# Optimization experiments

Hardware: AMD Instinct MI355X
Metric: run time of the kernel (lower is better)

The kernel has to match this reference:

```python
import jax, jax.numpy as jnp
import numpy as np

NUM_USERS = 100000
NUM_ITEMS = 50000
N = NUM_USERS + NUM_ITEMS
EMB = 64
NNZ = 4000000
B = 4096
GAMMA = 1.0
REG_LAMBDA = 1e-4
T_END = 1.0  # Euler step size: t = [0, 1]
EPS = 1e-12


def setup_inputs() -> dict:
    key = jax.random.key(0)
    ks = jax.random.split(key, 8)
    user = jax.random.randint(ks[0], (B,), 0, NUM_USERS)
    positive = jax.random.randint(ks[1], (B,), 0, NUM_ITEMS)
    negative = jax.random.randint(ks[2], (B,), 0, NUM_ITEMS)
    adj_rows = jax.random.randint(ks[3], (NNZ,), 0, N)
    adj_cols = jax.random.randint(ks[4], (NNZ,), 0, N)
    # normalized-adjacency-like small positive values
    adj_vals = jax.random.uniform(ks[5], (NNZ,), jnp.float32) * 1e-3
    user_emb = jax.random.normal(ks[6], (NUM_USERS, EMB), jnp.float32) * 0.1
    item_emb = jax.random.normal(ks[7], (NUM_ITEMS, EMB), jnp.float32) * 0.1
    return {
        "user": user, "positive": positive, "negative": negative,
        "adj_rows": adj_rows, "adj_cols": adj_cols, "adj_vals": adj_vals,
        "user_emb": user_emb, "item_emb": item_emb,
    }


def _normalize(x):
    return x * jax.lax.rsqrt(jnp.sum(x * x, axis=-1, keepdims=True) + EPS)


def _uniform_loss(x):
    # log mean_{i<j} exp(-2 * ||xn_i - xn_j||^2), xn = L2-normalized
    xn = _normalize(x)
    sq = jnp.maximum(2.0 - 2.0 * (xn @ xn.T), 0.0)  # [B, B] pairwise squared dist
    mask = jnp.triu(jnp.ones((x.shape[0], x.shape[0]), bool), k=1)
    vals = jnp.where(mask, jnp.exp(-2.0 * sq), 0.0)
    n_pairs = x.shape[0] * (x.shape[0] - 1) / 2.0
    return jnp.log(jnp.sum(vals) / n_pairs)


def reference(user, positive, negative, adj_rows, adj_cols, adj_vals, user_emb, item_emb):
    # ego embeddings: concat user/item tables -> [N, EMB]
    x = jnp.concatenate([user_emb, item_emb], axis=0)
    # sparse spmm: ax = A @ x (COO gather + segment reduce)
    ax = jax.ops.segment_sum(adj_vals[:, None] * x[adj_cols], adj_rows, num_segments=N)
    # ODEFunc f(t, x) = A@x + e with e = x0; one Euler step z1 = x0 + t*(A@x0 + x0)
    z = x + T_END * (ax + x)
    u_all, i_all = z[:NUM_USERS], z[NUM_USERS:]
    u = u_all[user]          # [B, EMB]
    i = i_all[positive]      # [B, EMB]
    # alignment loss on normalized embeddings
    un, inn = _normalize(u), _normalize(i)
    align = jnp.mean(jnp.sum((un - inn) ** 2, axis=-1))
    # uniformity loss
    uniform = GAMMA * (_uniform_loss(u) + _uniform_loss(i)) / 2.0
    # L2 reg on ego (pre-propagation) embeddings
    ego_u = user_emb[user]
    ego_i = item_emb[positive]
    reg = REG_LAMBDA * 0.5 * (jnp.sum(ego_u ** 2) + jnp.sum(ego_i ** 2)) / B
    return jnp.stack([align, uniform, reg])
```

## Files before the change

### kernel.cpp

```cpp
#include <hip/hip_runtime.h>
#include <math.h>

#define NUSERS 100000
#define NITEMS 50000
#define NN (NUSERS + NITEMS)
#define EMB 64
#define NNZ_ 4000000
#define BB 4096
#define NSLOT (2 * BB)
#define CAP 128
#define FSTR 32
#define BMW 4688
#define EPSN 1e-12f
#define NT128 32


typedef __attribute__((ext_vector_type(8))) short short8v;
typedef __attribute__((ext_vector_type(16))) float f32x16;

__device__ inline float wave_reduce_sum(float v) {
  #pragma unroll
  for (int off = 32; off >= 1; off >>= 1) v += __shfl_xor(v, off, 64);
  return v;
}

__device__ inline unsigned short f2bf(float f) {
  unsigned u = __float_as_uint(f);
  unsigned r = u + 0x7fffu + ((u >> 16) & 1u);
  return (unsigned short)(r >> 16);
}

__global__ __launch_bounds__(256) void lg_init(int* map, int* fillp, unsigned* bitmap) {
  int t = blockIdx.x * blockDim.x + threadIdx.x;
  if (t < NN) map[t] = -1;
  if (t < NSLOT * FSTR) fillp[t] = 0;
  if (t < BMW) bitmap[t] = 0u;
}

__global__ __launch_bounds__(256) void lg_mark(const int* __restrict__ user,
                                               const int* __restrict__ positive,
                                               int* __restrict__ map,
                                               unsigned* __restrict__ bitmap) {
  int t = blockIdx.x * blockDim.x + threadIdx.x;
  if (t >= 2 * BB) return;
  int row = (t < BB) ? user[t] : (NUSERS + positive[t - BB]);
  atomicCAS(&map[row], -1, t);
  atomicOr(&bitmap[row >> 5], 1u << (row & 31));
}

__device__ inline void lg_bin_one(int r, int c, float v, const unsigned* bm,
                                  const int* map, int* fillp, uint2* bins) {
  if ((bm[r >> 5] >> (r & 31)) & 1u) {
    int s = map[r];
    int pos = atomicAdd(&fillp[s * FSTR], 1);
    if (pos < CAP) {
      uint2 e; e.x = (unsigned)c; e.y = __float_as_uint(v);
      bins[(size_t)s * CAP + pos] = e;
    }
  }
}

__global__ __launch_bounds__(256) void lg_scan_bin(const int4* __restrict__ rows4,
                                                   const int4* __restrict__ cols4,
                                                   const float4* __restrict__ vals4,
                                                   const unsigned* __restrict__ bitmap,
                                                   const int* __restrict__ map,
                                                   int* __restrict__ fillp,
                                                   uint2* __restrict__ bins) {
  __shared__ unsigned bm[BMW];
  for (int i = threadIdx.x; i < BMW; i += 256) bm[i] = bitmap[i];
  __syncthreads();
  const int ngroups = NNZ_ / 4;
  for (int g = blockIdx.x * 256 + threadIdx.x; g < ngroups; g += gridDim.x * 256) {
    int4 r = rows4[g];
    int4 c = cols4[g];
    float4 v = vals4[g];
    lg_bin_one(r.x, c.x, v.x, bm, map, fillp, bins);
    lg_bin_one(r.y, c.y, v.y, bm, map, fillp, bins);
    lg_bin_one(r.z, c.z, v.z, bm, map, fillp, bins);
    lg_bin_one(r.w, c.w, v.w, bm, map, fillp, bins);
  }
}

__global__ __launch_bounds__(256) void lg_accum(const int* __restrict__ fillp,
                                                const uint2* __restrict__ bins,
                                                const float* __restrict__ uemb,
                                                const float* __restrict__ iemb,
                                                float* __restrict__ acc) {
  int w = (blockIdx.x * blockDim.x + threadIdx.x) >> 6;
  int lane = threadIdx.x & 63;
  if (w >= NSLOT) return;
  int n = min(fillp[w * FSTR], CAP);
  const uint2* bs = bins + (size_t)w * CAP;
  float a = 0.0f;
  int k = 0;
  for (; k + 4 <= n; k += 4) {
    uint2 e0 = bs[k];
    uint2 e1 = bs[k + 1];
    uint2 e2 = bs[k + 2];
    uint2 e3 = bs[k + 3];
    int c0 = (int)e0.x; float v0 = __uint_as_float(e0.y);
    int c1 = (int)e1.x; float v1 = __uint_as_float(e1.y);
    int c2 = (int)e2.x; float v2 = __uint_as_float(e2.y);
    int c3 = (int)e3.x; float v3 = __uint_as_float(e3.y);
    const float* x0 = (c0 < NUSERS) ? uemb + (size_t)c0 * EMB : iemb + (size_t)(c0 - NUSERS) * EMB;
    const float* x1 = (c1 < NUSERS) ? uemb + (size_t)c1 * EMB : iemb + (size_t)(c1 - NUSERS) * EMB;
    const float* x2 = (c2 < NUSERS) ? uemb + (size_t)c2 * EMB : iemb + (size_t)(c2 - NUSERS) * EMB;
    const float* x3 = (c3 < NUSERS) ? uemb + (size_t)c3 * EMB : iemb + (size_t)(c3 - NUSERS) * EMB;
    float f0 = x0[lane], f1 = x1[lane], f2 = x2[lane], f3 = x3[lane];
    a = fmaf(v0, f0, a);
    a = fmaf(v1, f1, a);
    a = fmaf(v2, f2, a);
    a = fmaf(v3, f3, a);
  }
  for (; k < n; ++k) {
    uint2 e0 = bs[k];
    int c0 = (int)e0.x; float v0 = __uint_as_float(e0.y);
    const float* x0 = (c0 < NUSERS) ? uemb + (size_t)c0 * EMB : iemb + (size_t)(c0 - NUSERS) * EMB;
    a = fmaf(v0, x0[lane], a);
  }
  acc[(size_t)w * EMB + lane] = a;
}

__global__ __launch_bounds__(256) void lg_prep(const int* __restrict__ user,
                                               const int* __restrict__ positive,
                                               const float* __restrict__ uemb,
                                               const float* __restrict__ iemb,
                                               const int* __restrict__ map,
                                               const float* __restrict__ acc,
                                               unsigned short* __restrict__ zub,
                                               unsigned short* __restrict__ zib,
                                               float* __restrict__ part_align,
                                               float* __restrict__ part_reg) {
  int w = (blockIdx.x * blockDim.x + threadIdx.x) >> 6;
  int lane = threadIdx.x & 63;
  if (w >= BB) return;
  int ru = user[w];
  int pi = positive[w];
  float eu = uemb[(size_t)ru * EMB + lane];
  float ei = iemb[(size_t)pi * EMB + lane];
  int su = map[ru];
  int si = map[NUSERS + pi];
  float zul = 2.0f * eu + acc[(size_t)su * EMB + lane];
  float zil = 2.0f * ei + acc[(size_t)si * EMB + lane];
  float nu = wave_reduce_sum(zul * zul);
  float ni = wave_reduce_sum(zil * zil);
  float un = zul * rsqrtf(nu + EPSN);
  float inn = zil * rsqrtf(ni + EPSN);
  zub[(size_t)w * EMB + lane] = f2bf(un);
  zib[(size_t)w * EMB + lane] = f2bf(inn);
  float d = un - inn;
  float align_b = wave_reduce_sum(d * d);
  float reg_b = wave_reduce_sum(eu * eu + ei * ei);
  if (lane == 0) {
    part_align[w] = align_b;
    part_reg[w] = reg_b;
  }
}

__global__ __launch_bounds__(256) void lg_gram_mfma(const unsigned short* __restrict__ zub,
                                                    const unsigned short* __restrict__ zib,
                                                    float* __restrict__ gpart) {
  int jb = blockIdx.x, ib = blockIdx.y, m = blockIdx.z;
  int bid = (m << 10) + (ib << 5) + jb;
  if (jb < ib) {
    if (threadIdx.x == 0) gpart[bid] = 0.0f;
    return;
  }
  const unsigned short* z = (m == 0) ? zub : zib;
  __shared__ float wsum[4];
  int t = threadIdx.x;
  int l = t & 63, w = t >> 6;
  int wr = w >> 1, wc = w & 1;
  int lr = l & 31;
  int koff = (l >> 5) * 8;
  const short8v* pa0 = (const short8v*)(z + (size_t)(ib * 128 + wr * 64 + lr) * EMB + koff);
  const short8v* pa1 = (const short8v*)(z + (size_t)(ib * 128 + wr * 64 + 32 + lr) * EMB + koff);
  const short8v* pb0 = (const short8v*)(z + (size_t)(jb * 128 + wc * 64 + lr) * EMB + koff);
  const short8v* pb1 = (const short8v*)(z + (size_t)(jb * 128 + wc * 64 + 32 + lr) * EMB + koff);
  f32x16 a00 = {}, a01 = {}, a10 = {}, a11 = {};
  #pragma unroll
  for (int ks = 0; ks < 4; ++ks) {
    short8v a0 = pa0[ks * 2];
    short8v a1 = pa1[ks * 2];
    short8v b0 = pb0[ks * 2];
    short8v b1 = pb1[ks * 2];
    a00 = __builtin_amdgcn_mfma_f32_32x32x16_bf16(a0, b0, a00, 0, 0, 0);
    a01 = __builtin_amdgcn_mfma_f32_32x32x16_bf16(a0, b1, a01, 0, 0, 0);
    a10 = __builtin_amdgcn_mfma_f32_32x32x16_bf16(a1, b0, a10, 0, 0, 0);
    a11 = __builtin_amdgcn_mfma_f32_32x32x16_bf16(a1, b1, a11, 0, 0, 0);
  }
  float s = 0.0f;
  #pragma unroll
  for (int e = 0; e < 16; ++e) {
    float v0 = a00[e], v1 = a01[e], v2 = a10[e], v3 = a11[e];
    s += __expf(-2.0f * fmaxf(fmaf(-2.0f, v0, 2.0f), 0.0f));
    s += __expf(-2.0f * fmaxf(fmaf(-2.0f, v1, 2.0f), 0.0f));
    s += __expf(-2.0f * fmaxf(fmaf(-2.0f, v2, 2.0f), 0.0f));
    s += __expf(-2.0f * fmaxf(fmaf(-2.0f, v3, 2.0f), 0.0f));
  }
  s = wave_reduce_sum(s);
  if (l == 0) wsum[w] = s;
  __syncthreads();
  if (t == 0) {
    float tot = wsum[0] + wsum[1] + wsum[2] + wsum[3];
    float wgt = (ib == jb) ? 1.0f : 2.0f;
    gpart[bid] = wgt * tot;
  }
}

__global__ __launch_bounds__(256) void lg_final(const float* __restrict__ part_align,
                                                const float* __restrict__ part_reg,
                                                const float* __restrict__ gpart,
                                                float* __restrict__ out) {
  __shared__ float red[4][4];
  int t = threadIdx.x;
  float sa = 0.0f, sr = 0.0f, su = 0.0f, si = 0.0f;
  for (int k = t; k < 4096; k += 256) {
    sa += part_align[k];
    sr += part_reg[k];
  }
  for (int k = t; k < 1024; k += 256) {
    su += gpart[k];
    si += gpart[1024 + k];
  }
  sa = wave_reduce_sum(sa);
  sr = wave_reduce_sum(sr);
  su = wave_reduce_sum(su);
  si = wave_reduce_sum(si);
  if ((t & 63) == 0) {
    int wid = t >> 6;
    red[wid][0] = sa; red[wid][1] = sr; red[wid][2] = su; red[wid][3] = si;
  }
  __syncthreads();
  if (t == 0) {
    float a = 0, r = 0, Su = 0, Si = 0;
    #pragma unroll
    for (int wv = 0; wv < 4; ++wv) {
      a += red[wv][0]; r += red[wv][1]; Su += red[wv][2]; Si += red[wv][3];
    }
    float align = a / (float)BB;
    float reg = 1e-4f * 0.5f * r / (float)BB;
    float npairs = (float)BB * (float)(BB - 1) * 0.5f;
    float tri_u = (Su - (float)BB) * 0.5f;
    float tri_i = (Si - (float)BB) * 0.5f;
    float Lu = logf(tri_u / npairs);
    float Li = logf(tri_i / npairs);
    out[0] = align;
    out[1] = 0.5f * (Lu + Li);
    out[2] = reg;
  }
}

extern "C" void kernel_launch(void* const* d_in, const int* in_sizes, int n_in,
                              void* d_out, int out_size, void* d_ws, size_t ws_size,
                              hipStream_t stream) {
  const int* user = (const int*)d_in[0];
  const int* positive = (const int*)d_in[1];
  const int* adj_rows = (const int*)d_in[3];
  const int* adj_cols = (const int*)d_in[4];
  const float* adj_vals = (const float*)d_in[5];
  const float* uemb = (const float*)d_in[6];
  const float* iemb = (const float*)d_in[7];

  char* ws = (char*)d_ws;
  int* map = (int*)(ws);
  int* fillp = (int*)(ws + (1u << 20));
  uint2* bins = (uint2*)(ws + (2u << 20));
  float* acc = (float*)(ws + (10u << 20));
  unsigned short* zub = (unsigned short*)(ws + (12u << 20));
  unsigned short* zib = (unsigned short*)(ws + (12u << 20) + (512u << 10));
  float* part_align = (float*)(ws + (13u << 20));
  float* part_reg = (float*)(ws + (13u << 20) + (16u << 10));
  float* gpart = (float*)(ws + (13u << 20) + (32u << 10));
  unsigned* bitmap = (unsigned*)(ws + (13u << 20) + (64u << 10));
  float* out = (float*)d_out;

  lg_init<<<dim3(1024), dim3(256), 0, stream>>>(map, fillp, bitmap);
  lg_mark<<<dim3(32), dim3(256), 0, stream>>>(user, positive, map, bitmap);
  lg_scan_bin<<<dim3(2048), dim3(256), 0, stream>>>(
      (const int4*)adj_rows, (const int4*)adj_cols, (const float4*)adj_vals,
      bitmap, map, fillp, bins);
  lg_accum<<<dim3(NSLOT / 4), dim3(256), 0, stream>>>(fillp, bins, uemb, iemb, acc);
  lg_prep<<<dim3(1024), dim3(256), 0, stream>>>(user, positive, uemb, iemb, map,
                                                acc, zub, zib, part_align, part_reg);
  lg_gram_mfma<<<dim3(NT128, NT128, 2), dim3(256), 0, stream>>>(zub, zib, gpart);
  lg_final<<<dim3(1), dim3(256), 0, stream>>>(part_align, part_reg, gpart, out);
}
```

Measured before the change: 71.79 us.

## Scan only row indices when binning; gather cols/vals later; enlarge Gram tiles

The binning scan now streams only adj_rows and stores the edge index for each matching entry. The later accumulate kernel gathers the column and value for those few edges, which removes two full 16MB streams from the scan. The Gram kernel moves to 256x256 upper-triangle tiles with 512 threads, indexed over 136 triangle blocks so no blocks launch only to exit. The cost is an extra dependent indirect load per edge in the accumulate step and fewer, larger Gram blocks.

```diff
diff --git a/kernel.cpp b/kernel.cpp
--- a/kernel.cpp
+++ b/kernel.cpp
@@ -12,7 +12,9 @@
 #define FSTR 32
 #define BMW 4688
 #define EPSN 1e-12f
-#define NT128 32
+#define BT 256
+#define NTB 16
+#define NTRI 136
 
 
 typedef __attribute__((ext_vector_type(8))) short short8v;
@@ -48,42 +50,38 @@
   atomicOr(&bitmap[row >> 5], 1u << (row & 31));
 }
 
-__device__ inline void lg_bin_one(int r, int c, float v, const unsigned* bm,
-                                  const int* map, int* fillp, uint2* bins) {
+__device__ inline void lg_bin_one(int r, int k, const unsigned* bm,
+                                  const int* map, int* fillp, unsigned* binsk) {
   if ((bm[r >> 5] >> (r & 31)) & 1u) {
     int s = map[r];
     int pos = atomicAdd(&fillp[s * FSTR], 1);
-    if (pos < CAP) {
-      uint2 e; e.x = (unsigned)c; e.y = __float_as_uint(v);
-      bins[(size_t)s * CAP + pos] = e;
-    }
+    if (pos < CAP) binsk[(size_t)s * CAP + pos] = (unsigned)k;
   }
 }
 
 __global__ __launch_bounds__(256) void lg_scan_bin(const int4* __restrict__ rows4,
-                                                   const int4* __restrict__ cols4,
-                                                   const float4* __restrict__ vals4,
                                                    const unsigned* __restrict__ bitmap,
                                                    const int* __restrict__ map,
                                                    int* __restrict__ fillp,
-                                                   uint2* __restrict__ bins) {
+                                                   unsigned* __restrict__ binsk) {
   __shared__ unsigned bm[BMW];
   for (int i = threadIdx.x; i < BMW; i += 256) bm[i] = bitmap[i];
   __syncthreads();
   const int ngroups = NNZ_ / 4;
   for (int g = blockIdx.x * 256 + threadIdx.x; g < ngroups; g += gridDim.x * 256) {
     int4 r = rows4[g];
-    int4 c = cols4[g];
-    float4 v = vals4[g];
-    lg_bin_one(r.x, c.x, v.x, bm, map, fillp, bins);
-    lg_bin_one(r.y, c.y, v.y, bm, map, fillp, bins);
-    lg_bin_one(r.z, c.z, v.z, bm, map, fillp, bins);
-    lg_bin_one(r.w, c.w, v.w, bm, map, fillp, bins);
+    int kb = g * 4;
+    lg_bin_one(r.x, kb + 0, bm, map, fillp, binsk);
+    lg_bin_one(r.y, kb + 1, bm, map, fillp, binsk);
+    lg_bin_one(r.z, kb + 2, bm, map, fillp, binsk);
+    lg_bin_one(r.w, kb + 3, bm, map, fillp, binsk);
   }
 }
 
 __global__ __launch_bounds__(256) void lg_accum(const int* __restrict__ fillp,
-                                                const uint2* __restrict__ bins,
+                                                const unsigned* __restrict__ binsk,
+                                                const int* __restrict__ cols,
+                                                const float* __restrict__ vals,
                                                 const float* __restrict__ uemb,
                                                 const float* __restrict__ iemb,
                                                 float* __restrict__ acc) {
@@ -91,18 +89,15 @@
   int lane = threadIdx.x & 63;
   if (w >= NSLOT) return;
   int n = min(fillp[w * FSTR], CAP);
-  const uint2* bs = bins + (size_t)w * CAP;
+  const unsigned* bs = binsk + (size_t)w * CAP;
   float a = 0.0f;
   int k = 0;
   for (; k + 4 <= n; k += 4) {
-    uint2 e0 = bs[k];
-    uint2 e1 = bs[k + 1];
-    uint2 e2 = bs[k + 2];
-    uint2 e3 = bs[k + 3];
-    int c0 = (int)e0.x; float v0 = __uint_as_float(e0.y);
-    int c1 = (int)e1.x; float v1 = __uint_as_float(e1.y);
-    int c2 = (int)e2.x; float v2 = __uint_as_float(e2.y);
-    int c3 = (int)e3.x; float v3 = __uint_as_float(e3.y);
+    unsigned k0 = bs[k], k1 = bs[k + 1], k2 = bs[k + 2], k3 = bs[k + 3];
+    int c0 = cols[k0]; float v0 = vals[k0];
+    int c1 = cols[k1]; float v1 = vals[k1];
+    int c2 = cols[k2]; float v2 = vals[k2];
+    int c3 = cols[k3]; float v3 = vals[k3];
     const float* x0 = (c0 < NUSERS) ? uemb + (size_t)c0 * EMB : iemb + (size_t)(c0 - NUSERS) * EMB;
     const float* x1 = (c1 < NUSERS) ? uemb + (size_t)c1 * EMB : iemb + (size_t)(c1 - NUSERS) * EMB;
     const float* x2 = (c2 < NUSERS) ? uemb + (size_t)c2 * EMB : iemb + (size_t)(c2 - NUSERS) * EMB;
@@ -114,8 +109,8 @@
     a = fmaf(v3, f3, a);
   }
   for (; k < n; ++k) {
-    uint2 e0 = bs[k];
-    int c0 = (int)e0.x; float v0 = __uint_as_float(e0.y);
+    unsigned k0 = bs[k];
+    int c0 = cols[k0]; float v0 = vals[k0];
     const float* x0 = (c0 < NUSERS) ? uemb + (size_t)c0 * EMB : iemb + (size_t)(c0 - NUSERS) * EMB;
     a = fmaf(v0, x0[lane], a);
   }
@@ -158,54 +153,68 @@
   }
 }
 
-__global__ __launch_bounds__(256) void lg_gram_mfma(const unsigned short* __restrict__ zub,
+__global__ __launch_bounds__(512) void lg_gram_mfma(const unsigned short* __restrict__ zub,
                                                     const unsigned short* __restrict__ zib,
                                                     float* __restrict__ gpart) {
-  int jb = blockIdx.x, ib = blockIdx.y, m = blockIdx.z;
-  int bid = (m << 10) + (ib << 5) + jb;
-  if (jb < ib) {
-    if (threadIdx.x == 0) gpart[bid] = 0.0f;
-    return;
-  }
+  int L = blockIdx.x, m = blockIdx.y;
+  int ib = 0, rem = L;
+  while (rem >= NTB - ib) { rem -= NTB - ib; ++ib; }
+  int jb = ib + rem;
   const unsigned short* z = (m == 0) ? zub : zib;
-  __shared__ float wsum[4];
+  __shared__ float wsum[8];
   int t = threadIdx.x;
   int l = t & 63, w = t >> 6;
   int wr = w >> 1, wc = w & 1;
   int lr = l & 31;
   int koff = (l >> 5) * 8;
-  const short8v* pa0 = (const short8v*)(z + (size_t)(ib * 128 + wr * 64 + lr) * EMB + koff);
-  const short8v* pa1 = (const short8v*)(z + (size_t)(ib * 128 + wr * 64 + 32 + lr) * EMB + koff);
-  const short8v* pb0 = (const short8v*)(z + (size_t)(jb * 128 + wc * 64 + lr) * EMB + koff);
-  const short8v* pb1 = (const short8v*)(z + (size_t)(jb * 128 + wc * 64 + 32 + lr) * EMB + koff);
-  f32x16 a00 = {}, a01 = {}, a10 = {}, a11 = {};
+  int arow = ib * BT + wr * 64;
+  int bcol = jb * BT + wc * 128;
+  const short8v* pa0 = (const short8v*)(z + (size_t)(arow + lr) * EMB + koff);
+  const short8v* pa1 = (const short8v*)(z + (size_t)(arow + 32 + lr) * EMB + koff);
+  const short8v* pb0 = (const short8v*)(z + (size_t)(bcol + lr) * EMB + koff);
+  const short8v* pb1 = (const short8v*)(z + (size_t)(bcol + 32 + lr) * EMB + koff);
+  const short8v* pb2 = (const short8v*)(z + (size_t)(bcol + 64 + lr) * EMB + koff);
+  const short8v* pb3 = (const short8v*)(z + (size_t)(bcol + 96 + lr) * EMB + koff);
+  f32x16 c00 = {}, c01 = {}, c02 = {}, c03 = {};
+  f32x16 c10 = {}, c11 = {}, c12 = {}, c13 = {};
   #pragma unroll
   for (int ks = 0; ks < 4; ++ks) {
     short8v a0 = pa0[ks * 2];
     short8v a1 = pa1[ks * 2];
     short8v b0 = pb0[ks * 2];
     short8v b1 = pb1[ks * 2];
-    a00 = __builtin_amdgcn_mfma_f32_32x32x16_bf16(a0, b0, a00, 0, 0, 0);
-    a01 = __builtin_amdgcn_mfma_f32_32x32x16_bf16(a0, b1, a01, 0, 0, 0);
-    a10 = __builtin_amdgcn_mfma_f32_32x32x16_bf16(a1, b0, a10, 0, 0, 0);
-    a11 = __builtin_amdgcn_mfma_f32_32x32x16_bf16(a1, b1, a11, 0, 0, 0);
+    short8v b2 = pb2[ks * 2];
+    short8v b3 = pb3[ks * 2];
+    c00 = __builtin_amdgcn_mfma_f32_32x32x16_bf16(a0, b0, c00, 0, 0, 0);
+    c01 = __builtin_amdgcn_mfma_f32_32x32x16_bf16(a0, b1, c01, 0, 0, 0);
+    c02 = __builtin_amdgcn_mfma_f32_32x32x16_bf16(a0, b2, c02, 0, 0, 0);
+    c03 = __builtin_amdgcn_mfma_f32_32x32x16_bf16(a0, b3, c03, 0, 0, 0);
+    c10 = __builtin_amdgcn_mfma_f32_32x32x16_bf16(a1, b0, c10, 0, 0, 0);
+    c11 = __builtin_amdgcn_mfma_f32_32x32x16_bf16(a1, b1, c11, 0, 0, 0);
+    c12 = __builtin_amdgcn_mfma_f32_32x32x16_bf16(a1, b2, c12, 0, 0, 0);
+    c13 = __builtin_amdgcn_mfma_f32_32x32x16_bf16(a1, b3, c13, 0, 0, 0);
   }
   float s = 0.0f;
   #pragma unroll
   for (int e = 0; e < 16; ++e) {
-    float v0 = a00[e], v1 = a01[e], v2 = a10[e], v3 = a11[e];
-    s += __expf(-2.0f * fmaxf(fmaf(-2.0f, v0, 2.0f), 0.0f));
-    s += __expf(-2.0f * fmaxf(fmaf(-2.0f, v1, 2.0f), 0.0f));
-    s += __expf(-2.0f * fmaxf(fmaf(-2.0f, v2, 2.0f), 0.0f));
-    s += __expf(-2.0f * fmaxf(fmaf(-2.0f, v3, 2.0f), 0.0f));
+    s += __expf(-2.0f * fmaxf(fmaf(-2.0f, c00[e], 2.0f), 0.0f));
+    s += __expf(-2.0f * fmaxf(fmaf(-2.0f, c01[e], 2.0f), 0.0f));
+    s += __expf(-2.0f * fmaxf(fmaf(-2.0f, c02[e], 2.0f), 0.0f));
+    s += __expf(-2.0f * fmaxf(fmaf(-2.0f, c03[e], 2.0f), 0.0f));
+    s += __expf(-2.0f * fmaxf(fmaf(-2.0f, c10[e], 2.0f), 0.0f));
+    s += __expf(-2.0f * fmaxf(fmaf(-2.0f, c11[e], 2.0f), 0.0f));
+    s += __expf(-2.0f * fmaxf(fmaf(-2.0f, c12[e], 2.0f), 0.0f));
+    s += __expf(-2.0f * fmaxf(fmaf(-2.0f, c13[e], 2.0f), 0.0f));
   }
   s = wave_reduce_sum(s);
   if (l == 0) wsum[w] = s;
   __syncthreads();
   if (t == 0) {
-    float tot = wsum[0] + wsum[1] + wsum[2] + wsum[3];
+    float tot = 0.0f;
+    #pragma unroll
+    for (int i = 0; i < 8; ++i) tot += wsum[i];
     float wgt = (ib == jb) ? 1.0f : 2.0f;
-    gpart[bid] = wgt * tot;
+    gpart[m * NTRI + L] = wgt * tot;
   }
 }
 
@@ -220,9 +229,9 @@
     sa += part_align[k];
     sr += part_reg[k];
   }
-  for (int k = t; k < 1024; k += 256) {
-    su += gpart[k];
-    si += gpart[1024 + k];
+  if (t < NTRI) {
+    su = gpart[t];
+    si = gpart[NTRI + t];
   }
   sa = wave_reduce_sum(sa);
   sr = wave_reduce_sum(sr);
@@ -266,24 +275,24 @@
   char* ws = (char*)d_ws;
   int* map = (int*)(ws);
   int* fillp = (int*)(ws + (1u << 20));
-  uint2* bins = (uint2*)(ws + (2u << 20));
-  float* acc = (float*)(ws + (10u << 20));
-  unsigned short* zub = (unsigned short*)(ws + (12u << 20));
-  unsigned short* zib = (unsigned short*)(ws + (12u << 20) + (512u << 10));
-  float* part_align = (float*)(ws + (13u << 20));
-  float* part_reg = (float*)(ws + (13u << 20) + (16u << 10));
-  float* gpart = (float*)(ws + (13u << 20) + (32u << 10));
-  unsigned* bitmap = (unsigned*)(ws + (13u << 20) + (64u << 10));
+  unsigned* binsk = (unsigned*)(ws + (2u << 20));
+  float* acc = (float*)(ws + (6u << 20));
+  unsigned short* zub = (unsigned short*)(ws + (8u << 20));
+  unsigned short* zib = (unsigned short*)(ws + (8u << 20) + (512u << 10));
+  float* part_align = (float*)(ws + (9u << 20));
+  float* part_reg = (float*)(ws + (9u << 20) + (16u << 10));
+  float* gpart = (float*)(ws + (9u << 20) + (32u << 10));
+  unsigned* bitmap = (unsigned*)(ws + (9u << 20) + (64u << 10));
   float* out = (float*)d_out;
 
   lg_init<<<dim3(1024), dim3(256), 0, stream>>>(map, fillp, bitmap);
   lg_mark<<<dim3(32), dim3(256), 0, stream>>>(user, positive, map, bitmap);
-  lg_scan_bin<<<dim3(2048), dim3(256), 0, stream>>>(
-      (const int4*)adj_rows, (const int4*)adj_cols, (const float4*)adj_vals,
-      bitmap, map, fillp, bins);
-  lg_accum<<<dim3(NSLOT / 4), dim3(256), 0, stream>>>(fillp, bins, uemb, iemb, acc);
+  lg_scan_bin<<<dim3(1024), dim3(256), 0, stream>>>(
+      (const int4*)adj_rows, bitmap, map, fillp, binsk);
+  lg_accum<<<dim3(NSLOT / 4), dim3(256), 0, stream>>>(fillp, binsk, adj_cols,
+                                                      adj_vals, uemb, iemb, acc);
   lg_prep<<<dim3(1024), dim3(256), 0, stream>>>(user, positive, uemb, iemb, map,
                                                 acc, zub, zib, part_align, part_reg);
-  lg_gram_mfma<<<dim3(NT128, NT128, 2), dim3(256), 0, stream>>>(zub, zib, gpart);
+  lg_gram_mfma<<<dim3(NTRI, 2), dim3(512), 0, stream>>>(zub, zib, gpart);
   lg_final<<<dim3(1), dim3(256), 0, stream>>>(part_align, part_reg, gpart, out);
 }
```

After: 80.02 us. +11.5%, slower.

## Pack fill counters, unroll scan to two groups, launch only upper-triangle gram tiles

Applied to the files above, without the earlier changes.

Three changes. The per-slot fill counters are now densely packed rather than padded to 32 ints apart, which shrinks the init work but lets atomics on neighbouring slots share cache lines. The scan kernel drops its grid-stride loop: each thread loads at most two int4 groups up front and then bins them, exposing more loads in flight. The gram kernel launches only the 528 upper-triangle tiles per matrix, decoded from a linear index, instead of a full 32x32 grid where half the blocks exit early.

```diff
diff --git a/kernel.cpp b/kernel.cpp
--- a/kernel.cpp
+++ b/kernel.cpp
@@ -9,10 +9,10 @@
 #define BB 4096
 #define NSLOT (2 * BB)
 #define CAP 128
-#define FSTR 32
 #define BMW 4688
 #define EPSN 1e-12f
-#define NT128 32
+#define NT 32
+#define NTRI 528
 
 
 typedef __attribute__((ext_vector_type(8))) short short8v;
@@ -33,7 +33,7 @@
 __global__ __launch_bounds__(256) void lg_init(int* map, int* fillp, unsigned* bitmap) {
   int t = blockIdx.x * blockDim.x + threadIdx.x;
   if (t < NN) map[t] = -1;
-  if (t < NSLOT * FSTR) fillp[t] = 0;
+  if (t < NSLOT) fillp[t] = 0;
   if (t < BMW) bitmap[t] = 0u;
 }
 
@@ -52,7 +52,7 @@
                                   const int* map, int* fillp, uint2* bins) {
   if ((bm[r >> 5] >> (r & 31)) & 1u) {
     int s = map[r];
-    int pos = atomicAdd(&fillp[s * FSTR], 1);
+    int pos = atomicAdd(&fillp[s], 1);
     if (pos < CAP) {
       uint2 e; e.x = (unsigned)c; e.y = __float_as_uint(v);
       bins[(size_t)s * CAP + pos] = e;
@@ -70,15 +70,30 @@
   __shared__ unsigned bm[BMW];
   for (int i = threadIdx.x; i < BMW; i += 256) bm[i] = bitmap[i];
   __syncthreads();
-  const int ngroups = NNZ_ / 4;
-  for (int g = blockIdx.x * 256 + threadIdx.x; g < ngroups; g += gridDim.x * 256) {
-    int4 r = rows4[g];
-    int4 c = cols4[g];
-    float4 v = vals4[g];
-    lg_bin_one(r.x, c.x, v.x, bm, map, fillp, bins);
-    lg_bin_one(r.y, c.y, v.y, bm, map, fillp, bins);
-    lg_bin_one(r.z, c.z, v.z, bm, map, fillp, bins);
-    lg_bin_one(r.w, c.w, v.w, bm, map, fillp, bins);
+  const int STRIDE = 2048 * 256;
+  const int NG = NNZ_ / 4;
+  int g0 = blockIdx.x * 256 + threadIdx.x;
+  int g1 = g0 + STRIDE;
+  int4 r0 = rows4[g0];
+  int4 c0 = cols4[g0];
+  float4 v0 = vals4[g0];
+  bool has1 = (g1 < NG);
+  int4 r1 = {}, c1 = {};
+  float4 v1 = {};
+  if (has1) {
+    r1 = rows4[g1];
+    c1 = cols4[g1];
+    v1 = vals4[g1];
+  }
+  lg_bin_one(r0.x, c0.x, v0.x, bm, map, fillp, bins);
+  lg_bin_one(r0.y, c0.y, v0.y, bm, map, fillp, bins);
+  lg_bin_one(r0.z, c0.z, v0.z, bm, map, fillp, bins);
+  lg_bin_one(r0.w, c0.w, v0.w, bm, map, fillp, bins);
+  if (has1) {
+    lg_bin_one(r1.x, c1.x, v1.x, bm, map, fillp, bins);
+    lg_bin_one(r1.y, c1.y, v1.y, bm, map, fillp, bins);
+    lg_bin_one(r1.z, c1.z, v1.z, bm, map, fillp, bins);
+    lg_bin_one(r1.w, c1.w, v1.w, bm, map, fillp, bins);
   }
 }
 
@@ -90,7 +105,7 @@
   int w = (blockIdx.x * blockDim.x + threadIdx.x) >> 6;
   int lane = threadIdx.x & 63;
   if (w >= NSLOT) return;
-  int n = min(fillp[w * FSTR], CAP);
+  int n = min(fillp[w], CAP);
   const uint2* bs = bins + (size_t)w * CAP;
   float a = 0.0f;
   int k = 0;
@@ -161,12 +176,10 @@
 __global__ __launch_bounds__(256) void lg_gram_mfma(const unsigned short* __restrict__ zub,
                                                     const unsigned short* __restrict__ zib,
                                                     float* __restrict__ gpart) {
-  int jb = blockIdx.x, ib = blockIdx.y, m = blockIdx.z;
-  int bid = (m << 10) + (ib << 5) + jb;
-  if (jb < ib) {
-    if (threadIdx.x == 0) gpart[bid] = 0.0f;
-    return;
-  }
+  int L = blockIdx.x, m = blockIdx.y;
+  int ib = 0, rem = L;
+  while (rem >= NT - ib) { rem -= NT - ib; ++ib; }
+  int jb = ib + rem;
   const unsigned short* z = (m == 0) ? zub : zib;
   __shared__ float wsum[4];
   int t = threadIdx.x;
@@ -193,11 +206,10 @@
   float s = 0.0f;
   #pragma unroll
   for (int e = 0; e < 16; ++e) {
-    float v0 = a00[e], v1 = a01[e], v2 = a10[e], v3 = a11[e];
-    s += __expf(-2.0f * fmaxf(fmaf(-2.0f, v0, 2.0f), 0.0f));
-    s += __expf(-2.0f * fmaxf(fmaf(-2.0f, v1, 2.0f), 0.0f));
-    s += __expf(-2.0f * fmaxf(fmaf(-2.0f, v2, 2.0f), 0.0f));
-    s += __expf(-2.0f * fmaxf(fmaf(-2.0f, v3, 2.0f), 0.0f));
+    s += __expf(-2.0f * fmaxf(fmaf(-2.0f, a00[e], 2.0f), 0.0f));
+    s += __expf(-2.0f * fmaxf(fmaf(-2.0f, a01[e], 2.0f), 0.0f));
+    s += __expf(-2.0f * fmaxf(fmaf(-2.0f, a10[e], 2.0f), 0.0f));
+    s += __expf(-2.0f * fmaxf(fmaf(-2.0f, a11[e], 2.0f), 0.0f));
   }
   s = wave_reduce_sum(s);
   if (l == 0) wsum[w] = s;
@@ -205,7 +217,7 @@
   if (t == 0) {
     float tot = wsum[0] + wsum[1] + wsum[2] + wsum[3];
     float wgt = (ib == jb) ? 1.0f : 2.0f;
-    gpart[bid] = wgt * tot;
+    gpart[m * NTRI + L] = wgt * tot;
   }
 }
 
@@ -220,9 +232,9 @@
     sa += part_align[k];
     sr += part_reg[k];
   }
-  for (int k = t; k < 1024; k += 256) {
+  for (int k = t; k < NTRI; k += 256) {
     su += gpart[k];
-    si += gpart[1024 + k];
+    si += gpart[NTRI + k];
   }
   sa = wave_reduce_sum(sa);
   sr = wave_reduce_sum(sr);
@@ -284,6 +296,6 @@
   lg_accum<<<dim3(NSLOT / 4), dim3(256), 0, stream>>>(fillp, bins, uemb, iemb, acc);
   lg_prep<<<dim3(1024), dim3(256), 0, stream>>>(user, positive, uemb, iemb, map,
                                                 acc, zub, zib, part_align, part_reg);
-  lg_gram_mfma<<<dim3(NT128, NT128, 2), dim3(256), 0, stream>>>(zub, zib, gpart);
+  lg_gram_mfma<<<dim3(NTRI, 2), dim3(256), 0, stream>>>(zub, zib, gpart);
   lg_final<<<dim3(1), dim3(256), 0, stream>>>(part_align, part_reg, gpart, out);
 }
```

Result: faster. 67.29 us (-6.3%).
